# Kernel optimization log

Measured on AMD Instinct MI355X. Metric: run time of the kernel, lower is better.

## Reference

```python
import jax, jax.numpy as jnp
import numpy as np

D = 4096          # in = out features of the quantized linear
K = 128           # n_quantize (codebook size)
B, S = 4, 4096    # batch, seq_len


def setup_inputs() -> dict:
    key = jax.random.key(0)
    k1, k2, k3, k4 = jax.random.split(key, 4)
    x = jax.random.normal(k1, (B, S, D), dtype=jnp.float32)
    quantized_vectors = jax.random.normal(k2, (D, K), dtype=jnp.float32)
    assignments = jax.random.randint(k3, (D,), 0, K, dtype=jnp.int32)
    bias = jax.random.normal(k4, (D,), dtype=jnp.float32)
    return {"x": x, "quantized_vectors": quantized_vectors,
            "assignments": assignments, "bias": bias}


def reference(x, quantized_vectors, assignments, bias):
    orig_shape = x.shape
    x_flat = x.reshape(-1, quantized_vectors.shape[0])          # [T, D]
    # row-gather the codebook then skinny matmul: [T, D] @ [D, K] -> [T, K]
    gathered = jnp.take(quantized_vectors, assignments, axis=0)  # [D, K]
    qm = jnp.einsum('ij,jk->ik', x_flat, gathered)               # [T, K]
    # column gather back to D outputs, add bias
    out = jnp.take(qm, assignments, axis=1) + bias[None, :]      # [T, D]
    return out.reshape(orig_shape)
```

## Files before the change

### kernel.cpp

```cpp
#include <hip/hip_runtime.h>
#include <hip/hip_fp16.h>

#define DD 4096
#define KK 128
#define NPAIR 16
#define XL2 4112
#define QVC_OFF 24832

union H2 { unsigned int u; __half2 h; };

static __device__ __forceinline__ unsigned int pkh2(float lo, float hi) {
    H2 r; r.h = __floats2half2_rn(lo, hi); return r.u;
}

__global__ void vq_build(const float* __restrict__ qv,
                         const int* __restrict__ assign,
                         unsigned short* __restrict__ puT16,
                         float4* __restrict__ qvC) {
    const int tid = threadIdx.x;

    if (blockIdx.x == 1) {
        for (int idx = tid; idx < 4096; idx += 256) {
            const int c4 = idx >> 7;
            const int k  = idx & (KK - 1);
            float4 v;
            v.x = qv[(4 * c4 + 0) * KK + k];
            v.y = qv[(4 * c4 + 1) * KK + k];
            v.z = qv[(4 * c4 + 2) * KK + k];
            v.w = qv[(4 * c4 + 3) * KK + k];
            qvC[idx] = v;
        }
        return;
    }

    __shared__ int off[KK];
    if (tid < KK) off[tid] = 0;

    {
        uint4* pT = reinterpret_cast<uint4*>(puT16);
        const unsigned int s = 0x10001000u;
        const uint4 sv = make_uint4(s, s, s, s);
        #pragma unroll
        for (int j = 0; j < 4; ++j)
            pT[tid * 4 + j] = sv;
    }
    __syncthreads();

    for (int j = tid; j < DD; j += 256) {
        const int c  = assign[j];
        const int p  = atomicAdd(&off[c], 1);
        const int th = 2 * c + (p & 1);
        const int i  = p >> 1;
        const int jj = i >> 1;
        if (jj < NPAIR)
            puT16[(th * NPAIR + jj) * 2 + (i & 1)] = (unsigned short)j;
    }
}

__global__ __launch_bounds__(256, 4) void vq_main(
    const float* __restrict__ x,
    const int*   __restrict__ assign,
    const float* __restrict__ bias,
    const uint4* __restrict__ puT,
    const float4* __restrict__ qvC,
    float* __restrict__ out)
{
    __shared__ unsigned int xp[XL2];
    __shared__ float xs[2 * KK];
    __shared__ float qm2[2 * KK];

    const int t0  = blockIdx.x * 2;
    const int tid = threadIdx.x;

    {
        const float4* r0 = reinterpret_cast<const float4*>(x + (size_t)(t0 + 0) * DD);
        const float4* r1 = reinterpret_cast<const float4*>(x + (size_t)(t0 + 1) * DD);
        uint4* pa = reinterpret_cast<uint4*>(xp);
        #pragma unroll
        for (int i = 0; i < 4; ++i) {
            const int idx = tid + i * 256;
            const float4 a = r0[idx];
            const float4 b = r1[idx];
            uint4 wa;
            wa.x = pkh2(a.x, b.x); wa.y = pkh2(a.y, b.y);
            wa.z = pkh2(a.z, b.z); wa.w = pkh2(a.w, b.w);
            pa[idx] = wa;
        }
        if (tid == 0) xp[DD] = 0u;
    }
    __syncthreads();

    {
        uint4 P0, P1, P2, P3;
        const uint4* pT = puT + tid * 4;
        P0 = pT[0]; P1 = pT[1]; P2 = pT[2]; P3 = pT[3];

        float s0 = 0.f, s1 = 0.f;
        #define VQ_ACC(pp) do {                                   \
            H2 w0_, w1_;                                          \
            w0_.u = xp[(pp) & 0xFFFFu];                           \
            w1_.u = xp[(pp) >> 16];                               \
            s0 += __low2float(w0_.h)  + __low2float(w1_.h);       \
            s1 += __high2float(w0_.h) + __high2float(w1_.h);      \
        } while (0)
        VQ_ACC(P0.x); VQ_ACC(P0.y); VQ_ACC(P0.z); VQ_ACC(P0.w);
        VQ_ACC(P1.x); VQ_ACC(P1.y); VQ_ACC(P1.z); VQ_ACC(P1.w);
        VQ_ACC(P2.x); VQ_ACC(P2.y); VQ_ACC(P2.z); VQ_ACC(P2.w);
        VQ_ACC(P3.x); VQ_ACC(P3.y); VQ_ACC(P3.z); VQ_ACC(P3.w);
        #undef VQ_ACC

        s0 += __shfl_xor(s0, 1);
        s1 += __shfl_xor(s1, 1);
        if ((tid & 1) == 0) {
            const int c = tid >> 1;
            xs[c]      = s0;
            xs[KK + c] = s1;
        }
    }
    __syncthreads();

    {
        const int k = tid >> 1;
        const int h = tid & 1;
        const float4* xsf4 = reinterpret_cast<const float4*>(xs);
        float4 a0 = make_float4(0.f, 0.f, 0.f, 0.f);
        float4 a1 = make_float4(0.f, 0.f, 0.f, 0.f);
        #pragma unroll
        for (int c4 = 0; c4 < 16; ++c4) {
            const int cg = h * 16 + c4;
            const float4 q  = qvC[cg * KK + k];
            const float4 v0 = xsf4[cg];
            const float4 v1 = xsf4[32 + cg];
            a0.x += q.x * v0.x;  a0.y += q.y * v0.y;
            a0.z += q.z * v0.z;  a0.w += q.w * v0.w;
            a1.x += q.x * v1.x;  a1.y += q.y * v1.y;
            a1.z += q.z * v1.z;  a1.w += q.w * v1.w;
        }
        float r0 = (a0.x + a0.y) + (a0.z + a0.w);
        float r1 = (a1.x + a1.y) + (a1.z + a1.w);
        r0 += __shfl_xor(r0, 1);
        r1 += __shfl_xor(r1, 1);
        if (h == 0) {
            qm2[2 * k]     = r0;
            qm2[2 * k + 1] = r1;
        }
    }
    __syncthreads();

    {
        const int4*   a4   = reinterpret_cast<const int4*>(assign);
        const float4* b4   = reinterpret_cast<const float4*>(bias);
        const float2* qmf2 = reinterpret_cast<const float2*>(qm2);
        float4* o0 = reinterpret_cast<float4*>(out + (size_t)(t0 + 0) * DD);
        float4* o1 = reinterpret_cast<float4*>(out + (size_t)(t0 + 1) * DD);
        #pragma unroll
        for (int i = 0; i < 4; ++i) {
            const int idx = tid + i * 256;
            const int4   a = a4[idx];
            const float4 b = b4[idx];
            const float2 qx = qmf2[a.x];
            const float2 qy = qmf2[a.y];
            const float2 qz = qmf2[a.z];
            const float2 qw = qmf2[a.w];
            float4 s0, s1;
            s0.x = qx.x + b.x;  s1.x = qx.y + b.x;
            s0.y = qy.x + b.y;  s1.y = qy.y + b.y;
            s0.z = qz.x + b.z;  s1.z = qz.y + b.z;
            s0.w = qw.x + b.w;  s1.w = qw.y + b.w;
            o0[idx] = s0;
            o1[idx] = s1;
        }
    }
}

extern "C" void kernel_launch(void* const* d_in, const int* in_sizes, int n_in,
                              void* d_out, int out_size, void* d_ws, size_t ws_size,
                              hipStream_t stream) {
    const float* x      = (const float*)d_in[0];
    const float* qv     = (const float*)d_in[1];
    const int*   assign = (const int*)d_in[2];
    const float* bias   = (const float*)d_in[3];
    float*       out    = (float*)d_out;

    unsigned short* puT16 = (unsigned short*)d_ws;
    float4* qvC = (float4*)((char*)d_ws + QVC_OFF);

    const int T = in_sizes[0] / DD;

    vq_build<<<dim3(2), dim3(256), 0, stream>>>(qv, assign, puT16, qvC);
    vq_main<<<dim3(T / 2), dim3(256), 0, stream>>>(
        x, assign, bias, (const uint4*)puT16, qvC, out);
}
```

Before: 453.7 us.

## Process eight token pairs per block with register prefetch of next rows

```diff
diff --git a/kernel.cpp b/kernel.cpp
--- a/kernel.cpp
+++ b/kernel.cpp
@@ -6,6 +6,7 @@
 #define NPAIR 16
 #define XL2 4112
 #define QVC_OFF 24832
+#define PPB 8
 
 union H2 { unsigned int u; __half2 h; };
 
@@ -69,106 +70,136 @@
     __shared__ float xs[2 * KK];
     __shared__ float qm2[2 * KK];
 
-    const int t0  = blockIdx.x * 2;
-    const int tid = threadIdx.x;
-
-    {
-        const float4* r0 = reinterpret_cast<const float4*>(x + (size_t)(t0 + 0) * DD);
-        const float4* r1 = reinterpret_cast<const float4*>(x + (size_t)(t0 + 1) * DD);
-        uint4* pa = reinterpret_cast<uint4*>(xp);
+    const int tid   = threadIdx.x;
+    const int pair0 = blockIdx.x * PPB;
+
+    uint4 P0, P1, P2, P3;
+    {
+        const uint4* pT = puT + tid * 4;
+        P0 = pT[0]; P1 = pT[1]; P2 = pT[2]; P3 = pT[3];
+    }
+    int4   A[4];
+    float4 Bs[4];
+    {
+        const int4*   a4 = reinterpret_cast<const int4*>(assign);
+        const float4* b4 = reinterpret_cast<const float4*>(bias);
         #pragma unroll
         for (int i = 0; i < 4; ++i) {
-            const int idx = tid + i * 256;
-            const float4 a = r0[idx];
-            const float4 b = r1[idx];
-            uint4 wa;
-            wa.x = pkh2(a.x, b.x); wa.y = pkh2(a.y, b.y);
-            wa.z = pkh2(a.z, b.z); wa.w = pkh2(a.w, b.w);
-            pa[idx] = wa;
-        }
-        if (tid == 0) xp[DD] = 0u;
-    }
-    __syncthreads();
-
-    {
-        uint4 P0, P1, P2, P3;
-        const uint4* pT = puT + tid * 4;
-        P0 = pT[0]; P1 = pT[1]; P2 = pT[2]; P3 = pT[3];
-
-        float s0 = 0.f, s1 = 0.f;
-        #define VQ_ACC(pp) do {                                   \
-            H2 w0_, w1_;                                          \
-            w0_.u = xp[(pp) & 0xFFFFu];                           \
-            w1_.u = xp[(pp) >> 16];                               \
-            s0 += __low2float(w0_.h)  + __low2float(w1_.h);       \
-            s1 += __high2float(w0_.h) + __high2float(w1_.h);      \
-        } while (0)
-        VQ_ACC(P0.x); VQ_ACC(P0.y); VQ_ACC(P0.z); VQ_ACC(P0.w);
-        VQ_ACC(P1.x); VQ_ACC(P1.y); VQ_ACC(P1.z); VQ_ACC(P1.w);
-        VQ_ACC(P2.x); VQ_ACC(P2.y); VQ_ACC(P2.z); VQ_ACC(P2.w);
-        VQ_ACC(P3.x); VQ_ACC(P3.y); VQ_ACC(P3.z); VQ_ACC(P3.w);
-        #undef VQ_ACC
-
-        s0 += __shfl_xor(s0, 1);
-        s1 += __shfl_xor(s1, 1);
-        if ((tid & 1) == 0) {
-            const int c = tid >> 1;
-            xs[c]      = s0;
-            xs[KK + c] = s1;
-        }
-    }
-    __syncthreads();
-
-    {
-        const int k = tid >> 1;
-        const int h = tid & 1;
-        const float4* xsf4 = reinterpret_cast<const float4*>(xs);
-        float4 a0 = make_float4(0.f, 0.f, 0.f, 0.f);
-        float4 a1 = make_float4(0.f, 0.f, 0.f, 0.f);
-        #pragma unroll
-        for (int c4 = 0; c4 < 16; ++c4) {
-            const int cg = h * 16 + c4;
-            const float4 q  = qvC[cg * KK + k];
-            const float4 v0 = xsf4[cg];
-            const float4 v1 = xsf4[32 + cg];
-            a0.x += q.x * v0.x;  a0.y += q.y * v0.y;
-            a0.z += q.z * v0.z;  a0.w += q.w * v0.w;
-            a1.x += q.x * v1.x;  a1.y += q.y * v1.y;
-            a1.z += q.z * v1.z;  a1.w += q.w * v1.w;
-        }
-        float r0 = (a0.x + a0.y) + (a0.z + a0.w);
-        float r1 = (a1.x + a1.y) + (a1.z + a1.w);
-        r0 += __shfl_xor(r0, 1);
-        r1 += __shfl_xor(r1, 1);
-        if (h == 0) {
-            qm2[2 * k]     = r0;
-            qm2[2 * k + 1] = r1;
-        }
-    }
-    __syncthreads();
-
-    {
-        const int4*   a4   = reinterpret_cast<const int4*>(assign);
-        const float4* b4   = reinterpret_cast<const float4*>(bias);
-        const float2* qmf2 = reinterpret_cast<const float2*>(qm2);
-        float4* o0 = reinterpret_cast<float4*>(out + (size_t)(t0 + 0) * DD);
-        float4* o1 = reinterpret_cast<float4*>(out + (size_t)(t0 + 1) * DD);
+            A[i]  = a4[tid + i * 256];
+            Bs[i] = b4[tid + i * 256];
+        }
+    }
+
+    float4 RA[4], RB[4];
+    {
+        const float4* r0 = reinterpret_cast<const float4*>(x + (size_t)(2 * pair0 + 0) * DD);
+        const float4* r1 = reinterpret_cast<const float4*>(x + (size_t)(2 * pair0 + 1) * DD);
         #pragma unroll
         for (int i = 0; i < 4; ++i) {
-            const int idx = tid + i * 256;
-            const int4   a = a4[idx];
-            const float4 b = b4[idx];
-            const float2 qx = qmf2[a.x];
-            const float2 qy = qmf2[a.y];
-            const float2 qz = qmf2[a.z];
-            const float2 qw = qmf2[a.w];
-            float4 s0, s1;
-            s0.x = qx.x + b.x;  s1.x = qx.y + b.x;
-            s0.y = qy.x + b.y;  s1.y = qy.y + b.y;
-            s0.z = qz.x + b.z;  s1.z = qz.y + b.z;
-            s0.w = qw.x + b.w;  s1.w = qw.y + b.w;
-            o0[idx] = s0;
-            o1[idx] = s1;
+            RA[i] = r0[tid + i * 256];
+            RB[i] = r1[tid + i * 256];
+        }
+    }
+
+    for (int p = 0; p < PPB; ++p) {
+        const int t0 = 2 * (pair0 + p);
+
+        {
+            uint4* pa = reinterpret_cast<uint4*>(xp);
+            #pragma unroll
+            for (int i = 0; i < 4; ++i) {
+                uint4 w;
+                w.x = pkh2(RA[i].x, RB[i].x);
+                w.y = pkh2(RA[i].y, RB[i].y);
+                w.z = pkh2(RA[i].z, RB[i].z);
+                w.w = pkh2(RA[i].w, RB[i].w);
+                pa[tid + i * 256] = w;
+            }
+            if (tid == 0) xp[DD] = 0u;
+        }
+        if (p + 1 < PPB) {
+            const float4* r0 = reinterpret_cast<const float4*>(x + (size_t)(t0 + 2) * DD);
+            const float4* r1 = reinterpret_cast<const float4*>(x + (size_t)(t0 + 3) * DD);
+            #pragma unroll
+            for (int i = 0; i < 4; ++i) {
+                RA[i] = r0[tid + i * 256];
+                RB[i] = r1[tid + i * 256];
+            }
+        }
+        __syncthreads();
+
+        {
+            float s0 = 0.f, s1 = 0.f;
+            #define VQ_ACC(pp) do {                                   \
+                H2 w0_, w1_;                                          \
+                w0_.u = xp[(pp) & 0xFFFFu];                           \
+                w1_.u = xp[(pp) >> 16];                               \
+                s0 += __low2float(w0_.h)  + __low2float(w1_.h);       \
+                s1 += __high2float(w0_.h) + __high2float(w1_.h);      \
+            } while (0)
+            VQ_ACC(P0.x); VQ_ACC(P0.y); VQ_ACC(P0.z); VQ_ACC(P0.w);
+            VQ_ACC(P1.x); VQ_ACC(P1.y); VQ_ACC(P1.z); VQ_ACC(P1.w);
+            VQ_ACC(P2.x); VQ_ACC(P2.y); VQ_ACC(P2.z); VQ_ACC(P2.w);
+            VQ_ACC(P3.x); VQ_ACC(P3.y); VQ_ACC(P3.z); VQ_ACC(P3.w);
+            #undef VQ_ACC
+
+            s0 += __shfl_xor(s0, 1);
+            s1 += __shfl_xor(s1, 1);
+            if ((tid & 1) == 0) {
+                const int c = tid >> 1;
+                xs[c]      = s0;
+                xs[KK + c] = s1;
+            }
+        }
+        __syncthreads();
+
+        {
+            const int k = tid >> 1;
+            const int h = tid & 1;
+            const float4* xsf4 = reinterpret_cast<const float4*>(xs);
+            float4 a0 = make_float4(0.f, 0.f, 0.f, 0.f);
+            float4 a1 = make_float4(0.f, 0.f, 0.f, 0.f);
+            #pragma unroll
+            for (int c4 = 0; c4 < 16; ++c4) {
+                const int cg = h * 16 + c4;
+                const float4 q  = qvC[cg * KK + k];
+                const float4 v0 = xsf4[cg];
+                const float4 v1 = xsf4[32 + cg];
+                a0.x += q.x * v0.x;  a0.y += q.y * v0.y;
+                a0.z += q.z * v0.z;  a0.w += q.w * v0.w;
+                a1.x += q.x * v1.x;  a1.y += q.y * v1.y;
+                a1.z += q.z * v1.z;  a1.w += q.w * v1.w;
+            }
+            float r0 = (a0.x + a0.y) + (a0.z + a0.w);
+            float r1 = (a1.x + a1.y) + (a1.z + a1.w);
+            r0 += __shfl_xor(r0, 1);
+            r1 += __shfl_xor(r1, 1);
+            if (h == 0) {
+                qm2[2 * k]     = r0;
+                qm2[2 * k + 1] = r1;
+            }
+        }
+        __syncthreads();
+
+        {
+            const float2* qmf2 = reinterpret_cast<const float2*>(qm2);
+            float4* o0 = reinterpret_cast<float4*>(out + (size_t)(t0 + 0) * DD);
+            float4* o1 = reinterpret_cast<float4*>(out + (size_t)(t0 + 1) * DD);
+            #pragma unroll
+            for (int i = 0; i < 4; ++i) {
+                const int idx = tid + i * 256;
+                const float2 qx = qmf2[A[i].x];
+                const float2 qy = qmf2[A[i].y];
+                const float2 qz = qmf2[A[i].z];
+                const float2 qw = qmf2[A[i].w];
+                float4 s0, s1;
+                s0.x = qx.x + Bs[i].x;  s1.x = qx.y + Bs[i].x;
+                s0.y = qy.x + Bs[i].y;  s1.y = qy.y + Bs[i].y;
+                s0.z = qz.x + Bs[i].z;  s1.z = qz.y + Bs[i].z;
+                s0.w = qw.x + Bs[i].w;  s1.w = qw.y + Bs[i].w;
+                o0[idx] = s0;
+                o1[idx] = s1;
+            }
         }
     }
 }
@@ -188,6 +219,6 @@
     const int T = in_sizes[0] / DD;
 
     vq_build<<<dim3(2), dim3(256), 0, stream>>>(qv, assign, puT16, qvC);
-    vq_main<<<dim3(T / 2), dim3(256), 0, stream>>>(
+    vq_main<<<dim3(T / 2 / PPB), dim3(256), 0, stream>>>(
         x, assign, bias, (const uint4*)puT16, qvC, out);
 }
```

After: 823.9 us. 1.82x slower.
